# Kernel tuning notes

Hardware: AMD Instinct MI355X
Metric: run time of the kernel (lower is better)

## Reference

```python
import jax, jax.numpy as jnp
import numpy as np

HIDDEN = 4544
N_HEADS = 71
HEAD_DIM = 64
SEQ = 2048
ROPE_BASE = 10000.0


def _rope_cos_sin(seq_len, dim, base=ROPE_BASE):
    inv_freq = 1.0 / (base ** (jnp.arange(0, dim, 2, dtype=jnp.float32) / dim))
    t = jnp.arange(seq_len, dtype=jnp.float32)
    freqs = jnp.einsum('i,j->ij', t, inv_freq)          # [s, dim/2]
    emb = jnp.concatenate([freqs, freqs], axis=-1)      # [s, dim]
    return jnp.cos(emb), jnp.sin(emb)


def _rotate_half(x):
    x1, x2 = jnp.split(x, 2, axis=-1)
    return jnp.concatenate([-x2, x1], axis=-1)


def _apply_rope(x, cos, sin):
    # x: [..., s, d]; cos/sin: [s, d] broadcast over leading dims
    return x * cos + _rotate_half(x) * sin


def setup_inputs() -> dict:
    key = jax.random.key(0)
    k1, k2, k3 = jax.random.split(key, 3)
    hidden_states = jax.random.normal(k1, (1, 1, SEQ, HIDDEN), dtype=jnp.float32) * 0.02
    qkv_weight = jax.random.normal(k2, ((N_HEADS + 2) * HEAD_DIM, HIDDEN), dtype=jnp.float32) * 0.02
    dense_weight = jax.random.normal(k3, (HIDDEN, HIDDEN), dtype=jnp.float32) * 0.02
    # causal additive mask, same construction as the torch module (triu of -1e5)
    mask = jnp.triu(jnp.full((SEQ, SEQ), -100000.0, dtype=jnp.float32), k=1)[None, None]
    return {
        'hidden_states': hidden_states,
        'qkv_weight': qkv_weight,
        'dense_weight': dense_weight,
        'attention_mask': mask,
    }


def reference(hidden_states, qkv_weight, dense_weight, attention_mask):
    b = hidden_states.shape[0]
    s = hidden_states.shape[2]
    x = hidden_states[:, 0]                                   # [b, s, H]

    # fused QKV projection (no bias): [b, s, (nH+2)*d]
    fused = jnp.einsum('bsh,oh->bso', x, qkv_weight)

    q = fused[..., : N_HEADS * HEAD_DIM]
    q = q.reshape(b, s, N_HEADS, HEAD_DIM).transpose(0, 2, 1, 3)   # [b, nH, s, d]
    k = fused[..., N_HEADS * HEAD_DIM : (N_HEADS + 1) * HEAD_DIM]  # [b, s, d] (single KV head, MQA)
    v = fused[..., (N_HEADS + 1) * HEAD_DIM :]                     # [b, s, d]

    cos, sin = _rope_cos_sin(s, HEAD_DIM)
    q = _apply_rope(q, cos, sin)
    k = _apply_rope(k, cos, sin)

    scale = 1.0 / np.sqrt(HEAD_DIM).astype(np.float32)
    scores = jnp.einsum('bhqd,bkd->bhqk', q, k) * scale            # [b, nH, s, s]
    scores = scores + attention_mask
    attn = jax.nn.softmax(scores, axis=-1)
    out = jnp.einsum('bhqk,bkd->bhqd', attn, v)                    # [b, nH, s, d]

    out = out.transpose(0, 2, 1, 3).reshape(b, s, N_HEADS * HEAD_DIM)  # concat heads
    out = jnp.einsum('bsh,oh->bso', out, dense_weight)             # dense projection
    return out[:, None]                                            # [b, 1, s, H]
```

## Files before the change

### kernel.cpp

```cpp
#include <hip/hip_runtime.h>

#define SEQ     2048
#define HIDDEN  4544
#define NHEAD   71
#define HD      64
#define QKV_OUT 4672

typedef __bf16    bf16;
typedef _Float16  f16;
typedef __bf16    bf16x8 __attribute__((ext_vector_type(8)));
typedef __bf16    bf16x4 __attribute__((ext_vector_type(4)));
typedef _Float16  f16x4  __attribute__((ext_vector_type(4)));
typedef float     f32x4  __attribute__((ext_vector_type(4)));

__device__ inline void gl2lds16(const void* g, void* ldsbase) {
  __builtin_amdgcn_global_load_lds(
      (const __attribute__((address_space(1))) unsigned int*)g,
      (__attribute__((address_space(3))) unsigned int*)ldsbase,
      16, 0, 0);
}

__global__ void cvt_f32_bf16_k(const float* __restrict__ in, bf16* __restrict__ out, int n4) {
  int i = blockIdx.x * blockDim.x + threadIdx.x;
  if (i >= n4) return;
  float4 f = ((const float4*)in)[i];
  bf16x4 o;
  o[0] = (bf16)f.x; o[1] = (bf16)f.y; o[2] = (bf16)f.z; o[3] = (bf16)f.w;
  *(bf16x4*)(out + (size_t)i * 4) = o;
}

__global__ __launch_bounds__(256) void gemm_bt_k(const bf16* __restrict__ A,
                                                 const bf16* __restrict__ B,
                                                 float* __restrict__ C,
                                                 int K, int Nmat, int ldc) {
  __shared__ bf16 lA[2][128 * 32];
  __shared__ bf16 lB[2][128 * 32];
  const int t = threadIdx.x;
  const int lane = t & 63, w = t >> 6;
  const int m0 = blockIdx.x * 128, n0 = blockIdx.y * 128;
  const int wm = (w >> 1) * 64, wn = (w & 1) * 64;
  const int qi = lane & 15, grp = lane >> 4;

  const int r0 = t >> 2;
  const int c0 = (t & 3) * 8;
  const bf16* gA0 = A + (size_t)(m0 + r0) * K + c0;
  const bf16* gA1 = A + (size_t)(m0 + 64 + r0) * K + c0;
  int bR0 = n0 + r0;      if (bR0 >= Nmat) bR0 = Nmat - 1;
  int bR1 = n0 + 64 + r0; if (bR1 >= Nmat) bR1 = Nmat - 1;
  const bf16* gB0 = B + (size_t)bR0 * K + c0;
  const bf16* gB1 = B + (size_t)bR1 * K + c0;
  bf16* lA00 = &lA[0][0] + w * 512;
  bf16* lA01 = &lA[0][2048] + w * 512;
  bf16* lA10 = &lA[1][0] + w * 512;
  bf16* lA11 = &lA[1][2048] + w * 512;
  bf16* lB00 = &lB[0][0] + w * 512;
  bf16* lB01 = &lB[0][2048] + w * 512;
  bf16* lB10 = &lB[1][0] + w * 512;
  bf16* lB11 = &lB[1][2048] + w * 512;

  f32x4 acc[4][4] = {};
  for (int k0 = 0; k0 < K; k0 += 64) {
    __syncthreads();
    gl2lds16(gA0 + k0,      lA00);
    gl2lds16(gA1 + k0,      lA01);
    gl2lds16(gA0 + k0 + 32, lA10);
    gl2lds16(gA1 + k0 + 32, lA11);
    gl2lds16(gB0 + k0,      lB00);
    gl2lds16(gB1 + k0,      lB01);
    gl2lds16(gB0 + k0 + 32, lB10);
    gl2lds16(gB1 + k0 + 32, lB11);
    __syncthreads();
#pragma unroll
    for (int half = 0; half < 2; ++half) {
      bf16x8 af[4], bfv[4];
#pragma unroll
      for (int i = 0; i < 4; ++i)
        af[i] = *(const bf16x8*)&lA[half][(wm + i * 16 + qi) * 32 + grp * 8];
#pragma unroll
      for (int i = 0; i < 4; ++i)
        bfv[i] = *(const bf16x8*)&lB[half][(wn + i * 16 + qi) * 32 + grp * 8];
#pragma unroll
      for (int i = 0; i < 4; ++i)
#pragma unroll
        for (int j = 0; j < 4; ++j)
          acc[i][j] = __builtin_amdgcn_mfma_f32_16x16x32_bf16(af[i], bfv[j], acc[i][j], 0, 0, 0);
    }
  }

#pragma unroll
  for (int i = 0; i < 4; ++i) {
    const int row = m0 + wm + i * 16 + grp * 4;
#pragma unroll
    for (int j = 0; j < 4; ++j) {
      const int col = n0 + wn + j * 16 + qi;
      if (col < Nmat) {
#pragma unroll
        for (int r = 0; r < 4; ++r)
          C[(size_t)(row + r) * ldc + col] = acc[i][j][r];
      }
    }
  }
}

__global__ __launch_bounds__(256) void rope_q_k(const float* __restrict__ fused,
                                                bf16* __restrict__ Qb,
                                                float* __restrict__ cs_tab,
                                                float* __restrict__ sn_tab) {
  const int s = blockIdx.x, t = threadIdx.x;
  __shared__ float cs[64], sn[64];
  if (t < 64) {
    int i = t & 31;
    double invf = pow(10000.0, -(double)i / 32.0);
    double ang = (double)s * invf;
    float c = (float)cos(ang), n = (float)sin(ang);
    cs[t] = c; sn[t] = n;
    cs_tab[s * 64 + t] = c;
    sn_tab[s * 64 + t] = n;
  }
  __syncthreads();
  const float* row = fused + (size_t)s * QKV_OUT;
  for (int e = t; e < HIDDEN; e += 256) {
    int d = e & 63;
    float x = row[e], xp = row[e ^ 32];
    float rot = (d < 32) ? -xp : xp;
    Qb[(size_t)s * HIDDEN + e] = (bf16)((x * cs[d] + rot * sn[d]) * 0.125f);
  }
}

__global__ __launch_bounds__(64) void kvprep_k(const float* __restrict__ fused,
                                               const float* __restrict__ cs_tab,
                                               const float* __restrict__ sn_tab,
                                               bf16* __restrict__ Kf,
                                               f16* __restrict__ Vf) {
  const int t16 = blockIdx.x, lane = threadIdx.x;
  const int qi = lane & 15, grp = lane >> 4;
  const int s = t16 * 16 + qi;
  const float* krow = fused + (size_t)s * QKV_OUT + NHEAD * 64;
  const float* cs = cs_tab + s * 64;
  const float* sn = sn_tab + s * 64;
#pragma unroll
  for (int half = 0; half < 2; ++half) {
    bf16x8 o;
    const int d0 = half * 32 + grp * 8;
#pragma unroll
    for (int j = 0; j < 8; ++j) {
      int d = d0 + j;
      float x = krow[d], xp = krow[d ^ 32];
      float rot = (d < 32) ? -xp : xp;
      o[j] = (bf16)(x * cs[d] + rot * sn[d]);
    }
    *(bf16x8*)&Kf[(t16 * 2 + half) * 512 + lane * 8] = o;
  }
#pragma unroll
  for (int tt = 0; tt < 4; ++tt) {
    f16x4 o;
#pragma unroll
    for (int j = 0; j < 4; ++j)
      o[j] = (f16)fused[(size_t)(t16 * 16 + grp * 4 + j) * QKV_OUT + (NHEAD + 1) * 64 + tt * 16 + qi];
    *(f16x4*)&Vf[t16 * 1024 + tt * 256 + lane * 4] = o;
  }
}

__global__ __launch_bounds__(64) void attn_k(const bf16* __restrict__ Qb,
                                             const bf16* __restrict__ Kf,
                                             const f16*  __restrict__ Vf,
                                             bf16* __restrict__ Ao) {
  __shared__ float fl[2 * 16 * 68];
  const int h = blockIdx.y;
  const int b32 = gridDim.x - 1 - blockIdx.x;
  const int lane = threadIdx.x;
  const int qi = lane & 15, grp = lane >> 4;
  const int q0 = b32 * 32;
  const int lastT = b32 >> 1;

  bf16x8 qf[2][2];
#pragma unroll
  for (int qq = 0; qq < 2; ++qq) {
    const bf16* qb = Qb + (size_t)(q0 + qq * 16 + qi) * HIDDEN + h * 64 + grp * 8;
    qf[qq][0] = *(const bf16x8*)qb;
    qf[qq][1] = *(const bf16x8*)(qb + 32);
  }

  f32x4 o[2][4] = {};
  float l[2] = {0.f, 0.f};

  for (int kb = 0; kb <= lastT; ++kb) {
    const bf16* kfp = Kf + (size_t)kb * 4096 + lane * 8;
    bf16x8 kf[4][2];
#pragma unroll
    for (int kk = 0; kk < 4; ++kk) {
      kf[kk][0] = *(const bf16x8*)(kfp + kk * 1024);
      kf[kk][1] = *(const bf16x8*)(kfp + kk * 1024 + 512);
    }
    f32x4 s4[2][4];
#pragma unroll
    for (int qq = 0; qq < 2; ++qq)
#pragma unroll
      for (int kk = 0; kk < 4; ++kk) {
        f32x4 z = {};
        s4[qq][kk] = __builtin_amdgcn_mfma_f32_16x16x32_bf16(kf[kk][0], qf[qq][0], z, 0, 0, 0);
        s4[qq][kk] = __builtin_amdgcn_mfma_f32_16x16x32_bf16(kf[kk][1], qf[qq][1], s4[qq][kk], 0, 0, 0);
      }
    const f16* vfp = Vf + (size_t)kb * 4096 + lane * 4;
    f16x4 vf[4][4];
#pragma unroll
    for (int kk = 0; kk < 4; ++kk)
#pragma unroll
      for (int tt = 0; tt < 4; ++tt)
        vf[kk][tt] = *(const f16x4*)(vfp + kk * 1024 + tt * 256);

    if (kb == lastT) {
      const int dq = q0 - kb * 64 + qi;
#pragma unroll
      for (int qq = 0; qq < 2; ++qq)
#pragma unroll
        for (int kk = 0; kk < 4; ++kk)
#pragma unroll
          for (int r = 0; r < 4; ++r)
            if (kk * 16 + grp * 4 + r > dq + qq * 16) s4[qq][kk][r] = -1e30f;
    }
    f16x4 pf[2][4];
#pragma unroll
    for (int qq = 0; qq < 2; ++qq) {
      float ls = 0.f;
#pragma unroll
      for (int kk = 0; kk < 4; ++kk) {
        float p0 = __expf(s4[qq][kk][0]), p1 = __expf(s4[qq][kk][1]);
        float p2 = __expf(s4[qq][kk][2]), p3 = __expf(s4[qq][kk][3]);
        ls += (p0 + p1) + (p2 + p3);
        pf[qq][kk][0] = (f16)p0; pf[qq][kk][1] = (f16)p1;
        pf[qq][kk][2] = (f16)p2; pf[qq][kk][3] = (f16)p3;
      }
      l[qq] += ls;
    }
#pragma unroll
    for (int qq = 0; qq < 2; ++qq)
#pragma unroll
      for (int tt = 0; tt < 4; ++tt)
#pragma unroll
        for (int kk = 0; kk < 4; ++kk)
          o[qq][tt] = __builtin_amdgcn_mfma_f32_16x16x16f16(pf[qq][kk], vf[kk][tt], o[qq][tt], 0, 0, 0);
  }

#pragma unroll
  for (int qq = 0; qq < 2; ++qq) {
    float lq = l[qq];
    lq += __shfl_xor(lq, 16);
    lq += __shfl_xor(lq, 32);
    const float inv = 1.0f / lq;
    const float i0 = __shfl(inv, grp * 4 + 0);
    const float i1 = __shfl(inv, grp * 4 + 1);
    const float i2 = __shfl(inv, grp * 4 + 2);
    const float i3 = __shfl(inv, grp * 4 + 3);
    float* flq = fl + qq * 1088;
#pragma unroll
    for (int tt = 0; tt < 4; ++tt) {
      flq[(grp * 4 + 0) * 68 + tt * 16 + qi] = o[qq][tt][0] * i0;
      flq[(grp * 4 + 1) * 68 + tt * 16 + qi] = o[qq][tt][1] * i1;
      flq[(grp * 4 + 2) * 68 + tt * 16 + qi] = o[qq][tt][2] * i2;
      flq[(grp * 4 + 3) * 68 + tt * 16 + qi] = o[qq][tt][3] * i3;
    }
  }
  __syncthreads();
  const int row = lane >> 2, c0 = (lane & 3) * 16;
#pragma unroll
  for (int qq = 0; qq < 2; ++qq) {
    const float* flq = fl + qq * 1088;
    bf16x8 w0, w1;
#pragma unroll
    for (int j = 0; j < 8; ++j) {
      w0[j] = (bf16)flq[row * 68 + c0 + j];
      w1[j] = (bf16)flq[row * 68 + c0 + 8 + j];
    }
    bf16* ob = Ao + (size_t)(q0 + qq * 16 + row) * HIDDEN + h * 64 + c0;
    *(bf16x8*)ob = w0;
    *(bf16x8*)(ob + 8) = w1;
  }
}

extern "C" void kernel_launch(void* const* d_in, const int* in_sizes, int n_in,
                              void* d_out, int out_size, void* d_ws, size_t ws_size,
                              hipStream_t stream) {
  (void)in_sizes; (void)n_in; (void)out_size; (void)ws_size;
  const float* hs   = (const float*)d_in[0];
  const float* wqkv = (const float*)d_in[1];
  const float* wd   = (const float*)d_in[2];
  float* out = (float*)d_out;

  char* ws = (char*)d_ws;
  size_t off = 0;
  auto alloc = [&](size_t b) -> char* {
    char* p = ws + off;
    off += (b + 255) & ~(size_t)255;
    return p;
  };
  bf16* Xb     = (bf16*)alloc((size_t)SEQ * HIDDEN * 2);
  bf16* Wqb    = (bf16*)alloc((size_t)QKV_OUT * HIDDEN * 2);
  bf16* Wdb    = (bf16*)alloc((size_t)HIDDEN * HIDDEN * 2);
  float* fused = (float*)alloc((size_t)SEQ * QKV_OUT * 4);
  bf16* Qb     = (bf16*)alloc((size_t)SEQ * HIDDEN * 2);
  bf16* Kf     = (bf16*)alloc((size_t)(SEQ / 16) * 1024 * 2);
  f16*  Vf     = (f16*)alloc((size_t)(SEQ / 16) * 1024 * 2);
  float* cs_tab = (float*)alloc((size_t)SEQ * 64 * 4);
  float* sn_tab = (float*)alloc((size_t)SEQ * 64 * 4);
  bf16* Ao     = (bf16*)fused;

  {
    int n4 = SEQ * HIDDEN / 4;
    cvt_f32_bf16_k<<<(n4 + 255) / 256, 256, 0, stream>>>(hs, Xb, n4);
    n4 = QKV_OUT * HIDDEN / 4;
    cvt_f32_bf16_k<<<(n4 + 255) / 256, 256, 0, stream>>>(wqkv, Wqb, n4);
    n4 = HIDDEN * HIDDEN / 4;
    cvt_f32_bf16_k<<<(n4 + 255) / 256, 256, 0, stream>>>(wd, Wdb, n4);
  }
  gemm_bt_k<<<dim3(SEQ / 128, (QKV_OUT + 127) / 128), 256, 0, stream>>>(
      Xb, Wqb, fused, HIDDEN, QKV_OUT, QKV_OUT);
  rope_q_k<<<SEQ, 256, 0, stream>>>(fused, Qb, cs_tab, sn_tab);
  kvprep_k<<<SEQ / 16, 64, 0, stream>>>(fused, cs_tab, sn_tab, Kf, Vf);
  attn_k<<<dim3(SEQ / 32, NHEAD), 64, 0, stream>>>(Qb, Kf, Vf, Ao);
  gemm_bt_k<<<dim3(SEQ / 128, (HIDDEN + 127) / 128), 256, 0, stream>>>(
      Ao, Wdb, out, HIDDEN, HIDDEN, HIDDEN);
}
```

Measured before the change: 578.6 us.

## Replace GEMM with 256x256 tile, 8-wave, 4-stage pipelined LDS kernel

Replaces the 128x128 double-buffered GEMM with a 256x256-tile, 512-thread kernel. It uses a 4-slot LDS ring with prefetch two K-steps ahead, partial vmcnt waits, XOR-swizzled LDS layout to cut bank conflicts, and setprio around the MFMA bursts. Weight matrices are zero-padded during bf16 conversion so tiles never need row clamping. The grid shrinks to 8x19 and 8x18 blocks, which may underfill the 256 CUs, and LDS use grows to 128KB per block.

```diff
diff --git a/kernel.cpp b/kernel.cpp
--- a/kernel.cpp
+++ b/kernel.cpp
@@ -5,6 +5,8 @@
 #define NHEAD   71
 #define HD      64
 #define QKV_OUT 4672
+#define QKV_PAD 4864
+#define HID_PAD 4608
 
 typedef __bf16    bf16;
 typedef _Float16  f16;
@@ -20,79 +22,104 @@
       16, 0, 0);
 }
 
-__global__ void cvt_f32_bf16_k(const float* __restrict__ in, bf16* __restrict__ out, int n4) {
+__global__ void cvt_pad_k(const float* __restrict__ in, bf16* __restrict__ out,
+                          int ncols4, int nrows, int n4tot) {
   int i = blockIdx.x * blockDim.x + threadIdx.x;
-  if (i >= n4) return;
-  float4 f = ((const float4*)in)[i];
+  if (i >= n4tot) return;
+  int row = i / ncols4;
   bf16x4 o;
-  o[0] = (bf16)f.x; o[1] = (bf16)f.y; o[2] = (bf16)f.z; o[3] = (bf16)f.w;
+  if (row < nrows) {
+    float4 f = ((const float4*)in)[i];
+    o[0] = (bf16)f.x; o[1] = (bf16)f.y; o[2] = (bf16)f.z; o[3] = (bf16)f.w;
+  } else {
+    o[0] = o[1] = o[2] = o[3] = (bf16)0.f;
+  }
   *(bf16x4*)(out + (size_t)i * 4) = o;
 }
 
-__global__ __launch_bounds__(256) void gemm_bt_k(const bf16* __restrict__ A,
-                                                 const bf16* __restrict__ B,
-                                                 float* __restrict__ C,
-                                                 int K, int Nmat, int ldc) {
-  __shared__ bf16 lA[2][128 * 32];
-  __shared__ bf16 lB[2][128 * 32];
+__global__ __launch_bounds__(512) void gemm8p_k(const bf16* __restrict__ A,
+                                                const bf16* __restrict__ B,
+                                                float* __restrict__ C,
+                                                int K, int Nmat, int ldc) {
+  __shared__ bf16 lA[4][256 * 32];
+  __shared__ bf16 lB[4][256 * 32];
   const int t = threadIdx.x;
   const int lane = t & 63, w = t >> 6;
-  const int m0 = blockIdx.x * 128, n0 = blockIdx.y * 128;
-  const int wm = (w >> 1) * 64, wn = (w & 1) * 64;
   const int qi = lane & 15, grp = lane >> 4;
-
-  const int r0 = t >> 2;
-  const int c0 = (t & 3) * 8;
-  const bf16* gA0 = A + (size_t)(m0 + r0) * K + c0;
-  const bf16* gA1 = A + (size_t)(m0 + 64 + r0) * K + c0;
-  int bR0 = n0 + r0;      if (bR0 >= Nmat) bR0 = Nmat - 1;
-  int bR1 = n0 + 64 + r0; if (bR1 >= Nmat) bR1 = Nmat - 1;
-  const bf16* gB0 = B + (size_t)bR0 * K + c0;
-  const bf16* gB1 = B + (size_t)bR1 * K + c0;
-  bf16* lA00 = &lA[0][0] + w * 512;
-  bf16* lA01 = &lA[0][2048] + w * 512;
-  bf16* lA10 = &lA[1][0] + w * 512;
-  bf16* lA11 = &lA[1][2048] + w * 512;
-  bf16* lB00 = &lB[0][0] + w * 512;
-  bf16* lB01 = &lB[0][2048] + w * 512;
-  bf16* lB10 = &lB[1][0] + w * 512;
-  bf16* lB11 = &lB[1][2048] + w * 512;
-
-  f32x4 acc[4][4] = {};
-  for (int k0 = 0; k0 < K; k0 += 64) {
-    __syncthreads();
-    gl2lds16(gA0 + k0,      lA00);
-    gl2lds16(gA1 + k0,      lA01);
-    gl2lds16(gA0 + k0 + 32, lA10);
-    gl2lds16(gA1 + k0 + 32, lA11);
-    gl2lds16(gB0 + k0,      lB00);
-    gl2lds16(gB1 + k0,      lB01);
-    gl2lds16(gB0 + k0 + 32, lB10);
-    gl2lds16(gB1 + k0 + 32, lB11);
-    __syncthreads();
-#pragma unroll
-    for (int half = 0; half < 2; ++half) {
-      bf16x8 af[4], bfv[4];
-#pragma unroll
-      for (int i = 0; i < 4; ++i)
-        af[i] = *(const bf16x8*)&lA[half][(wm + i * 16 + qi) * 32 + grp * 8];
-#pragma unroll
-      for (int i = 0; i < 4; ++i)
-        bfv[i] = *(const bf16x8*)&lB[half][(wn + i * 16 + qi) * 32 + grp * 8];
-#pragma unroll
-      for (int i = 0; i < 4; ++i)
-#pragma unroll
-        for (int j = 0; j < 4; ++j)
-          acc[i][j] = __builtin_amdgcn_mfma_f32_16x16x32_bf16(af[i], bfv[j], acc[i][j], 0, 0, 0);
-    }
-  }
-
-#pragma unroll
-  for (int i = 0; i < 4; ++i) {
-    const int row = m0 + wm + i * 16 + grp * 4;
+  const int wm = w >> 2, wn = w & 3;
+  const int m0 = blockIdx.x * 256, n0 = blockIdx.y * 256;
+
+  const int srow  = t >> 2;
+  const int sk8   = ((t & 3) ^ (srow & 3)) * 8;
+  const bf16* gA = A + (size_t)(m0 + srow) * K + sk8;
+  const bf16* gB = B + (size_t)(n0 + srow) * K + sk8;
+  const size_t halfR = (size_t)128 * K;
+
+  const int NK = K >> 5;
+  const int xsl = ((grp ^ (qi & 3)) * 8);
+
+  f32x4 acc[8][4] = {};
+  bf16x8 bfr[4];
+
+  {
+    gl2lds16(gA,               &lA[0][w * 512]);
+    gl2lds16(gA + halfR,       &lA[0][4096 + w * 512]);
+    gl2lds16(gB,               &lB[0][w * 512]);
+    gl2lds16(gB + halfR,       &lB[0][4096 + w * 512]);
+    gl2lds16(gA + 32,          &lA[1][w * 512]);
+    gl2lds16(gA + halfR + 32,  &lA[1][4096 + w * 512]);
+    gl2lds16(gB + 32,          &lB[1][w * 512]);
+    gl2lds16(gB + halfR + 32,  &lB[1][4096 + w * 512]);
+  }
+
+  for (int kt = 0; kt < NK; ++kt) {
+    const int s = kt & 3;
+    const int sn = (kt + 2) & 3;
+    const int kf = (kt + 2 < NK ? kt + 2 : NK - 1) << 5;
+
+    gl2lds16(gA + kf,          &lA[sn][w * 512]);
+    gl2lds16(gA + halfR + kf,  &lA[sn][4096 + w * 512]);
+    asm volatile("s_waitcnt vmcnt(6)" ::: "memory");
+    __builtin_amdgcn_s_barrier();
+    asm volatile("" ::: "memory");
+    bf16x8 afr[4];
+#pragma unroll
+    for (int i = 0; i < 4; ++i)
+      afr[i] = *(const bf16x8*)&lA[s][(wm * 128 + i * 16 + qi) * 32 + xsl];
+#pragma unroll
+    for (int j = 0; j < 4; ++j)
+      bfr[j] = *(const bf16x8*)&lB[s][(wn * 64 + j * 16 + qi) * 32 + xsl];
+    __builtin_amdgcn_s_setprio(1);
+#pragma unroll
+    for (int i = 0; i < 4; ++i)
+#pragma unroll
+      for (int j = 0; j < 4; ++j)
+        acc[i][j] = __builtin_amdgcn_mfma_f32_16x16x32_bf16(afr[i], bfr[j], acc[i][j], 0, 0, 0);
+    __builtin_amdgcn_s_setprio(0);
+    __builtin_amdgcn_s_barrier();
+
+    gl2lds16(gB + kf,          &lB[sn][w * 512]);
+    gl2lds16(gB + halfR + kf,  &lB[sn][4096 + w * 512]);
+    __builtin_amdgcn_s_barrier();
+#pragma unroll
+    for (int i = 0; i < 4; ++i)
+      afr[i] = *(const bf16x8*)&lA[s][(wm * 128 + (i + 4) * 16 + qi) * 32 + xsl];
+    __builtin_amdgcn_s_setprio(1);
+#pragma unroll
+    for (int i = 0; i < 4; ++i)
+#pragma unroll
+      for (int j = 0; j < 4; ++j)
+        acc[i + 4][j] = __builtin_amdgcn_mfma_f32_16x16x32_bf16(afr[i], bfr[j], acc[i + 4][j], 0, 0, 0);
+    __builtin_amdgcn_s_setprio(0);
+    __builtin_amdgcn_s_barrier();
+  }
+
+#pragma unroll
+  for (int i = 0; i < 8; ++i) {
+    const int row = m0 + wm * 128 + i * 16 + grp * 4;
 #pragma unroll
     for (int j = 0; j < 4; ++j) {
-      const int col = n0 + wn + j * 16 + qi;
+      const int col = n0 + wn * 64 + j * 16 + qi;
       if (col < Nmat) {
 #pragma unroll
         for (int r = 0; r < 4; ++r)
@@ -295,8 +322,8 @@
     return p;
   };
   bf16* Xb     = (bf16*)alloc((size_t)SEQ * HIDDEN * 2);
-  bf16* Wqb    = (bf16*)alloc((size_t)QKV_OUT * HIDDEN * 2);
-  bf16* Wdb    = (bf16*)alloc((size_t)HIDDEN * HIDDEN * 2);
+  bf16* Wqb    = (bf16*)alloc((size_t)QKV_PAD * HIDDEN * 2);
+  bf16* Wdb    = (bf16*)alloc((size_t)HID_PAD * HIDDEN * 2);
   float* fused = (float*)alloc((size_t)SEQ * QKV_OUT * 4);
   bf16* Qb     = (bf16*)alloc((size_t)SEQ * HIDDEN * 2);
   bf16* Kf     = (bf16*)alloc((size_t)(SEQ / 16) * 1024 * 2);
@@ -305,19 +332,20 @@
   float* sn_tab = (float*)alloc((size_t)SEQ * 64 * 4);
   bf16* Ao     = (bf16*)fused;
 
+  const int NC4 = HIDDEN / 4;
   {
-    int n4 = SEQ * HIDDEN / 4;
-    cvt_f32_bf16_k<<<(n4 + 255) / 256, 256, 0, stream>>>(hs, Xb, n4);
-    n4 = QKV_OUT * HIDDEN / 4;
-    cvt_f32_bf16_k<<<(n4 + 255) / 256, 256, 0, stream>>>(wqkv, Wqb, n4);
-    n4 = HIDDEN * HIDDEN / 4;
-    cvt_f32_bf16_k<<<(n4 + 255) / 256, 256, 0, stream>>>(wd, Wdb, n4);
-  }
-  gemm_bt_k<<<dim3(SEQ / 128, (QKV_OUT + 127) / 128), 256, 0, stream>>>(
+    int n4 = SEQ * NC4;
+    cvt_pad_k<<<(n4 + 255) / 256, 256, 0, stream>>>(hs, Xb, NC4, SEQ, n4);
+    n4 = QKV_PAD * NC4;
+    cvt_pad_k<<<(n4 + 255) / 256, 256, 0, stream>>>(wqkv, Wqb, NC4, QKV_OUT, n4);
+    n4 = HID_PAD * NC4;
+    cvt_pad_k<<<(n4 + 255) / 256, 256, 0, stream>>>(wd, Wdb, NC4, HIDDEN, n4);
+  }
+  gemm8p_k<<<dim3(SEQ / 256, QKV_PAD / 256), 512, 0, stream>>>(
       Xb, Wqb, fused, HIDDEN, QKV_OUT, QKV_OUT);
   rope_q_k<<<SEQ, 256, 0, stream>>>(fused, Qb, cs_tab, sn_tab);
   kvprep_k<<<SEQ / 16, 64, 0, stream>>>(fused, cs_tab, sn_tab, Kf, Vf);
   attn_k<<<dim3(SEQ / 32, NHEAD), 64, 0, stream>>>(Qb, Kf, Vf, Ao);
-  gemm_bt_k<<<dim3(SEQ / 128, (HIDDEN + 127) / 128), 256, 0, stream>>>(
+  gemm8p_k<<<dim3(SEQ / 256, HID_PAD / 256), 512, 0, stream>>>(
       Ao, Wdb, out, HIDDEN, HIDDEN, HIDDEN);
 }
```

New measurement: 752.3 us. 30.0% more time.

## Swizzle GEMM block order and widen V fragment loads to 16 bytes

Applied to the files above, without the earlier changes.

The GEMM kernel remaps its linear workgroup index with a stride-8 interleave, so that workgroups dispatched close together share A or B tiles in cache. The V fragment layout written by the prep kernel is changed to pack two 16-wide column groups per lane into one 8-element f16 vector. This lets the attention kernel fetch V with 16-byte loads instead of 8-byte loads. The swizzle assumes the workgroup count is divisible by 8, and the V layout change has to match between the producer and the consumer kernels.

```diff
diff --git a/kernel.cpp b/kernel.cpp
--- a/kernel.cpp
+++ b/kernel.cpp
@@ -11,6 +11,7 @@
 typedef __bf16    bf16x8 __attribute__((ext_vector_type(8)));
 typedef __bf16    bf16x4 __attribute__((ext_vector_type(4)));
 typedef _Float16  f16x4  __attribute__((ext_vector_type(4)));
+typedef _Float16  f16x8  __attribute__((ext_vector_type(8)));
 typedef float     f32x4  __attribute__((ext_vector_type(4)));
 
 __device__ inline void gl2lds16(const void* g, void* ldsbase) {
@@ -37,7 +38,14 @@
   __shared__ bf16 lB[2][128 * 32];
   const int t = threadIdx.x;
   const int lane = t & 63, w = t >> 6;
-  const int m0 = blockIdx.x * 128, n0 = blockIdx.y * 128;
+
+  const int gx = gridDim.x;
+  const int nwg = gx * gridDim.y;
+  const int orig = blockIdx.y * gx + blockIdx.x;
+  const int swz = (orig & 7) * (nwg >> 3) + (orig >> 3);
+  const int m0 = (swz % gx) * 128;
+  const int n0 = (swz / gx) * 128;
+
   const int wm = (w >> 1) * 64, wn = (w & 1) * 64;
   const int qi = lane & 15, grp = lane >> 4;
 
@@ -152,12 +160,16 @@
     *(bf16x8*)&Kf[(t16 * 2 + half) * 512 + lane * 8] = o;
   }
 #pragma unroll
-  for (int tt = 0; tt < 4; ++tt) {
-    f16x4 o;
-#pragma unroll
-    for (int j = 0; j < 4; ++j)
-      o[j] = (f16)fused[(size_t)(t16 * 16 + grp * 4 + j) * QKV_OUT + (NHEAD + 1) * 64 + tt * 16 + qi];
-    *(f16x4*)&Vf[t16 * 1024 + tt * 256 + lane * 4] = o;
+  for (int p = 0; p < 2; ++p) {
+    f16x8 o;
+#pragma unroll
+    for (int h = 0; h < 2; ++h) {
+      const int tt = p * 2 + h;
+#pragma unroll
+      for (int j = 0; j < 4; ++j)
+        o[h * 4 + j] = (f16)fused[(size_t)(t16 * 16 + grp * 4 + j) * QKV_OUT + (NHEAD + 1) * 64 + tt * 16 + qi];
+    }
+    *(f16x8*)&Vf[t16 * 1024 + p * 512 + lane * 8] = o;
   }
 }
 
@@ -201,13 +213,19 @@
         s4[qq][kk] = __builtin_amdgcn_mfma_f32_16x16x32_bf16(kf[kk][0], qf[qq][0], z, 0, 0, 0);
         s4[qq][kk] = __builtin_amdgcn_mfma_f32_16x16x32_bf16(kf[kk][1], qf[qq][1], s4[qq][kk], 0, 0, 0);
       }
-    const f16* vfp = Vf + (size_t)kb * 4096 + lane * 4;
+    const f16* vfp = Vf + (size_t)kb * 4096 + lane * 8;
     f16x4 vf[4][4];
 #pragma unroll
     for (int kk = 0; kk < 4; ++kk)
 #pragma unroll
-      for (int tt = 0; tt < 4; ++tt)
-        vf[kk][tt] = *(const f16x4*)(vfp + kk * 1024 + tt * 256);
+      for (int p = 0; p < 2; ++p) {
+        f16x8 v8 = *(const f16x8*)(vfp + kk * 1024 + p * 512);
+#pragma unroll
+        for (int j = 0; j < 4; ++j) {
+          vf[kk][2 * p][j]     = v8[j];
+          vf[kk][2 * p + 1][j] = v8[4 + j];
+        }
+      }
 
     if (kb == lastT) {
       const int dq = q0 - kb * 64 + qi;
```

Result: faster. 550.0 us (-4.9%).
